# Kernel tuning notes

Measured on AMD Instinct MI355X. Metric: run time of the kernel, lower is better.

Reference implementation:

```python
import jax, jax.numpy as jnp
import numpy as np

N_NODES = 100000
N_EDGES = 1600000
IN_DIM, HID_DIM, OUT_DIM = 256, 64, 64


def gcn_conv(x, src, dst, W, b, n_nodes):
    """PyG GCNConv: D^-1/2 (A + I) D^-1/2 X W + b (self-loops added, deg on dst)."""
    h = x @ W  # [N, D_out]
    ones = jnp.ones(src.shape[0], dtype=h.dtype)
    deg = jax.ops.segment_sum(ones, dst, num_segments=n_nodes) + 1.0  # +1 for self-loop
    dinv = jax.lax.rsqrt(deg)  # deg >= 1, always finite
    norm = dinv[src] * dinv[dst]  # [E]
    # neighbor aggregation (scatter-add) + self-loop contribution
    agg = jax.ops.segment_sum(h[src] * norm[:, None], dst, num_segments=n_nodes)
    agg = agg + h * (dinv * dinv)[:, None]
    return agg + b


def gcn_backbone(x, edge_index, W1, b1, W2, b2, n_nodes):
    src, dst = edge_index[0], edge_index[1]
    h = jax.nn.relu(gcn_conv(x, src, dst, W1, b1, n_nodes))
    h = gcn_conv(h, src, dst, W2, b2, n_nodes)
    return h


def zscore(h):
    # torch .std(0) is unbiased (ddof=1)
    return (h - h.mean(axis=0)) / jnp.std(h, axis=0, ddof=1)


def setup_inputs() -> dict:
    key = jax.random.key(0)
    k = jax.random.split(key, 8)
    x1 = jax.random.normal(k[0], (N_NODES, IN_DIM), dtype=jnp.float32)
    x2 = jax.random.normal(k[1], (N_NODES, IN_DIM), dtype=jnp.float32)
    edge_index1 = jax.random.randint(k[2], (2, N_EDGES), 0, N_NODES, dtype=jnp.int64)
    edge_index2 = jax.random.randint(k[3], (2, N_EDGES), 0, N_NODES, dtype=jnp.int64)
    W1 = jax.random.normal(k[4], (IN_DIM, HID_DIM), dtype=jnp.float32) * (1.0 / np.sqrt(IN_DIM))
    b1 = jnp.zeros((HID_DIM,), dtype=jnp.float32)
    W2 = jax.random.normal(k[5], (HID_DIM, OUT_DIM), dtype=jnp.float32) * (1.0 / np.sqrt(HID_DIM))
    b2 = jnp.zeros((OUT_DIM,), dtype=jnp.float32)
    return {"x1": x1, "edge_index1": edge_index1, "x2": x2, "edge_index2": edge_index2,
            "W1": W1, "b1": b1, "W2": W2, "b2": b2}


def reference(x1, edge_index1, x2, edge_index2, W1, b1, W2, b2):
    h1 = gcn_backbone(x1, edge_index1, W1, b1, W2, b2, N_NODES)
    h2 = gcn_backbone(x2, edge_index2, W1, b1, W2, b2, N_NODES)
    return zscore(h1), zscore(h2)
```

## Files before the change

kernel.cpp:

```cpp
#include <hip/hip_runtime.h>
#include <hip/hip_bf16.h>

#define HD 64
#define CH 8192
#define BKT_SHIFT 10
#define SRC_BITS 17
#define MAXBLK 256

typedef __attribute__((ext_vector_type(8))) short bf16x8;
typedef __attribute__((ext_vector_type(4))) float f32x4;

__device__ inline unsigned short f2bf(float x) {
  unsigned u = __float_as_uint(x);
  unsigned r = u + 0x7FFF + ((u >> 16) & 1);
  return (unsigned short)(r >> 16);
}
__device__ inline float bf2f(unsigned short h) {
  return __uint_as_float(((unsigned)h) << 16);
}

__global__ __launch_bounds__(256) void k_bin1(const int* __restrict__ src0,
                                              const int* __restrict__ dst0,
                                              const int* __restrict__ src1,
                                              const int* __restrict__ dst1,
                                              int* __restrict__ tmp,
                                              int* __restrict__ counts,
                                              int* __restrict__ offsets,
                                              int NB, int NBLK, int E) {
  __shared__ int hist[128];
  __shared__ int pref[128];
  __shared__ int lofs[128];
  __shared__ int stage[CH];
  const int g = blockIdx.x / NBLK;
  const int blk = blockIdx.x % NBLK;
  const int* __restrict__ src = g ? src1 : src0;
  const int* __restrict__ dst = g ? dst1 : dst0;
  int* __restrict__ tmpg = tmp + (size_t)g * NBLK * CH;
  int* __restrict__ cntg = counts + (size_t)g * NB * NBLK;
  int* __restrict__ offg = offsets + (size_t)g * NB * NBLK;
  const int e0 = blk * CH;
  const int len = min(CH, E - e0);
  const int t = threadIdx.x;

  for (int i = t; i < 128; i += 256) hist[i] = 0;
  __syncthreads();
  int dreg[CH / 256];
#pragma unroll
  for (int it = 0; it < CH / 256; ++it) {
    int i = t + it * 256;
    if (i < len) {
      int d = dst[e0 + i];
      dreg[it] = d;
      atomicAdd(&hist[d >> BKT_SHIFT], 1);
    }
  }
  __syncthreads();
  if (t < 128) pref[t] = hist[t];
  __syncthreads();
  for (int off = 1; off < 128; off <<= 1) {
    int v = 0;
    if (t < 128 && t >= off) v = pref[t - off];
    __syncthreads();
    if (t < 128) pref[t] += v;
    __syncthreads();
  }
  if (t < NB) {
    int ex = pref[t] - hist[t];
    lofs[t] = ex;
    cntg[t * NBLK + blk] = hist[t];
    offg[t * NBLK + blk] = ex;
  }
  __syncthreads();
#pragma unroll
  for (int it = 0; it < CH / 256; ++it) {
    int i = t + it * 256;
    if (i < len) {
      int d = dreg[it], s = src[e0 + i];
      int slot = atomicAdd(&lofs[d >> BKT_SHIFT], 1);
      stage[slot] = ((d & ((1 << BKT_SHIFT) - 1)) << SRC_BITS) | s;
    }
  }
  __syncthreads();
  int nv = len >> 2;
  for (int i = t; i < nv; i += 256) ((int4*)(tmpg + e0))[i] = ((const int4*)stage)[i];
  for (int i = (nv << 2) + t; i < len; i += 256) tmpg[e0 + i] = stage[i];
}

__global__ __launch_bounds__(128) void k_bscan(const int* __restrict__ counts,
                                               int* __restrict__ bucket_base,
                                               int* __restrict__ row_start,
                                               int NB, int NBLK, int N, int E) {
  __shared__ int sh[128];
  const int g = blockIdx.x;
  const int* __restrict__ cntg = counts + (size_t)g * NB * NBLK;
  int* __restrict__ bbg = bucket_base + g * (NB + 1);
  int* __restrict__ rsg = row_start + (size_t)g * (N + 1);
  int t = threadIdx.x;
  int v = 0;
  if (t < NB) {
    const int* p = cntg + t * NBLK;
    for (int i = 0; i < NBLK; ++i) v += p[i];
  }
  sh[t] = v;
  __syncthreads();
  for (int off = 1; off < 128; off <<= 1) {
    int x = (t >= off) ? sh[t - off] : 0;
    __syncthreads();
    sh[t] += x;
    __syncthreads();
  }
  if (t < NB) bbg[t] = sh[t] - v;
  if (t == 0) {
    bbg[NB] = E;
    rsg[N] = E;
  }
}

__global__ __launch_bounds__(1024) void k_bin2m(const int* __restrict__ tmp,
                                                const int* __restrict__ counts,
                                                const int* __restrict__ offsets,
                                                const int* __restrict__ bucket_base,
                                                int* __restrict__ row_start,
                                                float* __restrict__ dinv,
                                                int* __restrict__ recs, int N, int NB,
                                                int NBLK, int E) {
  __shared__ int h[1 << BKT_SHIFT];
  __shared__ int lcur[1 << BKT_SHIFT];
  __shared__ int scnt[MAXBLK], soff[MAXBLK];
  const int g = blockIdx.x / NB;
  const int b = blockIdx.x % NB;
  const int* __restrict__ tmpg = tmp + (size_t)g * NBLK * CH;
  const int* __restrict__ cntg = counts + (size_t)g * NB * NBLK;
  const int* __restrict__ offg = offsets + (size_t)g * NB * NBLK;
  const int* __restrict__ bbg = bucket_base + g * (NB + 1);
  int* __restrict__ rsg = row_start + (size_t)g * (N + 1);
  float* __restrict__ dig = dinv + (size_t)g * N;
  int* __restrict__ recg = recs + (size_t)g * E;
  const int t = threadIdx.x;
  const int node0 = b << BKT_SHIFT;
  const int lane = t & 63, w = t >> 6;

  h[t] = 0;
  for (int i = t; i < NBLK; i += 1024) {
    scnt[i] = cntg[b * NBLK + i];
    soff[i] = offg[b * NBLK + i];
  }
  __syncthreads();
  for (int blk = w; blk < NBLK; blk += 16) {
    int cnt = scnt[blk];
    const int* p = tmpg + blk * CH + soff[blk];
    for (int j = lane; j < cnt; j += 64) atomicAdd(&h[p[j] >> SRC_BITS], 1);
  }
  __syncthreads();
  int deg = h[t];
  __syncthreads();
  for (int off = 1; off < 1024; off <<= 1) {
    int x = (t >= off) ? h[t - off] : 0;
    __syncthreads();
    h[t] += x;
    __syncthreads();
  }
  int base = bbg[b] + h[t] - deg;
  lcur[t] = base;
  int n = node0 + t;
  if (n < N) {
    rsg[n] = base;
    dig[n] = rsqrtf((float)deg + 1.0f);
  }
  __syncthreads();
  for (int blk = w; blk < NBLK; blk += 16) {
    int cnt = scnt[blk];
    const int* p = tmpg + blk * CH + soff[blk];
    for (int j = lane; j < cnt; j += 64) {
      int rec = p[j];
      int d = rec >> SRC_BITS;
      int s = rec & ((1 << SRC_BITS) - 1);
      int slot = atomicAdd(&lcur[d], 1);
      recg[slot] = s;
    }
  }
}

template <int K, int A_BF16, int B_LO>
__global__ __launch_bounds__(512, 6) void k_gemm(const void* __restrict__ Xv0,
                                                 const void* __restrict__ Xv1,
                                                 const float* __restrict__ W,
                                                 unsigned short* __restrict__ Hb, int N,
                                                 int gPer) {
  constexpr int NKS = K / 32;
  __shared__ unsigned short sBhi[NKS * 4 * 64 * 8];
  __shared__ unsigned short sBlo[B_LO ? NKS * 4 * 64 * 8 : 8];
  const int tid = threadIdx.x;
  const int g = blockIdx.x / gPer;
  const int bblk = blockIdx.x % gPer;
  const void* __restrict__ Xv = g ? Xv1 : Xv0;

  for (int idx = tid; idx < K * 64; idx += 512) {
    int k = idx >> 6, c = idx & 63;
    float wval = W[idx];
    int ks = k >> 5, r = k & 31, h2 = r >> 3, j = r & 7;
    int f = c >> 4, r16c = c & 15;
    int pos = (((ks * 4 + f) * 64) + h2 * 16 + r16c) * 8 + j;
    unsigned short hi = f2bf(wval);
    sBhi[pos] = hi;
    if (B_LO) sBlo[pos] = f2bf(wval - bf2f(hi));
  }
  __syncthreads();

  const int lane = tid & 63;
  const int wv = tid >> 6;
  const int r16 = lane & 15;
  const int half = lane >> 4;
  const int row = bblk * 128 + wv * 16 + r16;

  f32x4 acc[4];
#pragma unroll
  for (int f = 0; f < 4; ++f) acc[f] = (f32x4){0.f, 0.f, 0.f, 0.f};

#pragma unroll
  for (int ks = 0; ks < NKS; ++ks) {
    bf16x8 ahi;
    if constexpr (A_BF16) {
      union { uint4 u; bf16x8 v; } au;
      au.u = make_uint4(0, 0, 0, 0);
      if (row < N)
        au.u = *(const uint4*)((const unsigned short*)Xv + (size_t)row * K + ks * 32 + half * 8);
      ahi = au.v;
    } else {
      float4 v0 = make_float4(0.f, 0.f, 0.f, 0.f), v1 = v0;
      if (row < N) {
        const float* xp = (const float*)Xv + (size_t)row * K + ks * 32 + half * 8;
        v0 = *(const float4*)xp;
        v1 = *(const float4*)(xp + 4);
      }
      union { __hip_bfloat162 h[4]; bf16x8 v; } cu;
      cu.h[0] = __float22bfloat162_rn(make_float2(v0.x, v0.y));
      cu.h[1] = __float22bfloat162_rn(make_float2(v0.z, v0.w));
      cu.h[2] = __float22bfloat162_rn(make_float2(v1.x, v1.y));
      cu.h[3] = __float22bfloat162_rn(make_float2(v1.z, v1.w));
      ahi = cu.v;
    }
#pragma unroll
    for (int f = 0; f < 4; ++f) {
      bf16x8 bh = *(const bf16x8*)&sBhi[(((ks * 4 + f) * 64) + lane) * 8];
      acc[f] = __builtin_amdgcn_mfma_f32_16x16x32_bf16(ahi, bh, acc[f], 0, 0, 0);
      if constexpr (B_LO) {
        bf16x8 bl = *(const bf16x8*)&sBlo[(((ks * 4 + f) * 64) + lane) * 8];
        acc[f] = __builtin_amdgcn_mfma_f32_16x16x32_bf16(ahi, bl, acc[f], 0, 0, 0);
      }
    }
  }

  const int orow0 = bblk * 128 + wv * 16 + half * 4;
#pragma unroll
  for (int f = 0; f < 4; ++f) {
#pragma unroll
    for (int rg = 0; rg < 4; ++rg) {
      int orow = orow0 + rg;
      if (orow < N) Hb[((size_t)g * N + orow) * HD + f * 16 + r16] = f2bf(acc[f][rg]);
    }
  }
}

template <int OUTBF16>
__global__ __launch_bounds__(256) void k_agg(const unsigned short* __restrict__ Hb,
                                             const int* __restrict__ recs,
                                             const int* __restrict__ row_start,
                                             const float* __restrict__ dinv,
                                             const float* __restrict__ bias,
                                             void* __restrict__ outv, int N, int E,
                                             int relu) {
  const int t = threadIdx.x;
  const int nglob = (blockIdx.x * blockDim.x + t) >> 4;
  const int lane16 = t & 15;
  if (nglob >= 2 * N) return;
  const int g = nglob >= N;
  const int node = nglob - g * N;
  const int* __restrict__ rsg = row_start + (size_t)g * (N + 1);
  const int* __restrict__ R = recs + (size_t)g * E;
  const float* __restrict__ dig = dinv + (size_t)g * N;
  const unsigned short* __restrict__ Hbg = Hb + (size_t)g * N * HD;

  const int c0 = lane16 * 4;
  float di = dig[node];
  float a0, a1, a2, a3;
  {
    uint2 h = *(const uint2*)&Hbg[(size_t)node * HD + c0];
    float dd = di * di;
    a0 = bf2f((unsigned short)(h.x & 0xffff)) * dd;
    a1 = bf2f((unsigned short)(h.x >> 16)) * dd;
    a2 = bf2f((unsigned short)(h.y & 0xffff)) * dd;
    a3 = bf2f((unsigned short)(h.y >> 16)) * dd;
  }
  const int beg = rsg[node], end = rsg[node + 1];
  int e = beg;
  for (; e + 8 <= end; e += 8) {
    int s[8];
    uint2 gg[8];
    float n[8];
#pragma unroll
    for (int j = 0; j < 8; ++j) s[j] = R[e + j];
#pragma unroll
    for (int j = 0; j < 8; ++j) {
      gg[j] = *(const uint2*)&Hbg[(size_t)s[j] * HD + c0];
      n[j] = dig[s[j]];
    }
#pragma unroll
    for (int j = 0; j < 8; ++j) {
      float nn = n[j] * di;
      a0 = fmaf(bf2f((unsigned short)(gg[j].x & 0xffff)), nn, a0);
      a1 = fmaf(bf2f((unsigned short)(gg[j].x >> 16)), nn, a1);
      a2 = fmaf(bf2f((unsigned short)(gg[j].y & 0xffff)), nn, a2);
      a3 = fmaf(bf2f((unsigned short)(gg[j].y >> 16)), nn, a3);
    }
  }
  for (; e < end; ++e) {
    int s = R[e];
    uint2 gg = *(const uint2*)&Hbg[(size_t)s * HD + c0];
    float nn = dig[s] * di;
    a0 = fmaf(bf2f((unsigned short)(gg.x & 0xffff)), nn, a0);
    a1 = fmaf(bf2f((unsigned short)(gg.x >> 16)), nn, a1);
    a2 = fmaf(bf2f((unsigned short)(gg.y & 0xffff)), nn, a2);
    a3 = fmaf(bf2f((unsigned short)(gg.y >> 16)), nn, a3);
  }
  float4 bv = *(const float4*)&bias[c0];
  a0 += bv.x; a1 += bv.y; a2 += bv.z; a3 += bv.w;
  if (relu) {
    a0 = fmaxf(a0, 0.f); a1 = fmaxf(a1, 0.f);
    a2 = fmaxf(a2, 0.f); a3 = fmaxf(a3, 0.f);
  }
  if (OUTBF16) {
    uint2 o;
    o.x = ((unsigned)f2bf(a1) << 16) | f2bf(a0);
    o.y = ((unsigned)f2bf(a3) << 16) | f2bf(a2);
    *(uint2*)&((unsigned short*)outv)[(size_t)nglob * HD + c0] = o;
  } else {
    *(float4*)&((float*)outv)[(size_t)nglob * HD + c0] = make_float4(a0, a1, a2, a3);
  }
}


__global__ void k_colstats(const float* __restrict__ H, float* __restrict__ stats, int N,
                           int gridPer) {
  __shared__ float ss[256], sq[256];
  const int g = blockIdx.x / gridPer;
  const int blk = blockIdx.x % gridPer;
  const float* __restrict__ Hg = H + (size_t)g * N * HD;
  float* __restrict__ st = stats + g * 128;
  int t = threadIdx.x;
  int col = t & 63, grp = t >> 6;
  float s = 0.f, q = 0.f;
  for (int row = blk * 4 + grp; row < N; row += gridPer * 4) {
    float v = Hg[(size_t)row * HD + col];
    s += v;
    q += v * v;
  }
  ss[t] = s;
  sq[t] = q;
  __syncthreads();
  if (t < 64) {
    s = ss[t] + ss[t + 64] + ss[t + 128] + ss[t + 192];
    q = sq[t] + sq[t + 64] + sq[t + 128] + sq[t + 192];
    atomicAdd(&st[t], s);
    atomicAdd(&st[64 + t], q);
  }
}

__global__ void k_normalize(float* __restrict__ H, const float* __restrict__ stats, int N) {
  int i = blockIdx.x * blockDim.x + threadIdx.x;
  int total = 2 * N * HD;
  if (i >= total) return;
  int col = i & 63;
  const float* st = stats + (i >= N * HD ? 128 : 0);
  float sum = st[col], sumsq = st[64 + col];
  float mean = sum / (float)N;
  float var = (sumsq - sum * sum / (float)N) / (float)(N - 1);
  float r = rsqrtf(var);
  H[i] = (H[i] - mean) * r;
}


extern "C" void kernel_launch(void* const* d_in, const int* in_sizes, int n_in,
                              void* d_out, int out_size, void* d_ws, size_t ws_size,
                              hipStream_t stream) {
  const int IN_DIM = 256;
  const float* X1 = (const float*)d_in[0];
  const float* X2 = (const float*)d_in[2];
  const int* EI1 = (const int*)d_in[1];
  const int* EI2 = (const int*)d_in[3];
  const float* W1 = (const float*)d_in[4];
  const float* b1 = (const float*)d_in[5];
  const float* W2 = (const float*)d_in[6];
  const float* b2 = (const float*)d_in[7];
  const int N = in_sizes[0] / IN_DIM;
  const int E = in_sizes[1] / 2;
  const int NB = (N + (1 << BKT_SHIFT) - 1) >> BKT_SHIFT;
  const int NBLK = (E + CH - 1) / CH;

  char* ws = (char*)d_ws;
  size_t off = 0;
  auto carve = [&](size_t bytes) -> char* {
    char* p = ws + off;
    off += (bytes + 255) & ~(size_t)255;
    return p;
  };
  unsigned short* Hb = (unsigned short*)carve((size_t)2 * N * HD * 2);
  int* tmp = (int*)carve((size_t)2 * NBLK * CH * 4);
  int* recs = (int*)carve((size_t)2 * E * 4);
  char* zero_base = carve(256 * 4);
  float* stats = (float*)zero_base;
  int* row_start = (int*)carve((size_t)2 * (N + 1) * 4);
  float* dinv = (float*)carve((size_t)2 * N * 4);
  int* bucket_base = (int*)carve((size_t)2 * (NB + 1) * 4);
  int* counts = (int*)carve((size_t)2 * NB * NBLK * 4);
  int* offsets = (int*)carve((size_t)2 * NB * NBLK * 4);
  unsigned short* bufAgg = (unsigned short*)d_out;
  (void)ws_size; (void)n_in; (void)out_size;

  const int T = 256;
  const int gPer1 = (N + 127) / 128;
  const int gPer2 = (2 * N + 127) / 128;
  const int gAgg = (2 * N * 16 + T - 1) / T;
  const int gCS = 512;
  const int gElem = (2 * N * HD + T - 1) / T;

  (void)hipMemsetAsync(zero_base, 0, 256 * 4, stream);
  k_bin1<<<2 * NBLK, T, 0, stream>>>(EI1, EI1 + E, EI2, EI2 + E, tmp, counts, offsets,
                                     NB, NBLK, E);
  k_bscan<<<2, 128, 0, stream>>>(counts, bucket_base, row_start, NB, NBLK, N, E);
  k_bin2m<<<2 * NB, 1024, 0, stream>>>(tmp, counts, offsets, bucket_base, row_start,
                                       dinv, recs, N, NB, NBLK, E);

  k_gemm<256, 0, 0><<<2 * gPer1, 512, 0, stream>>>(X1, X2, W1, Hb, N, gPer1);
  k_agg<1><<<gAgg, T, 0, stream>>>(Hb, recs, row_start, dinv, b1, bufAgg, N, E, 1);
  k_gemm<64, 1, 1><<<gPer2, 512, 0, stream>>>(bufAgg, bufAgg, W2, Hb, 2 * N, gPer2);
  k_agg<0><<<gAgg, T, 0, stream>>>(Hb, recs, row_start, dinv, b2, d_out, N, E, 0);

  k_colstats<<<2 * gCS, T, 0, stream>>>((float*)d_out, stats, N, gCS);
  k_normalize<<<gElem, T, 0, stream>>>((float*)d_out, stats, N);
}
```

Baseline: 364.4 us.

## Stage GEMM A-tiles into LDS via global_load_lds with XOR swizzle

The GEMM kernel now loads X rows straight into shared memory with the direct global-to-LDS load instruction, using coalesced 16-byte chunks and an XOR swizzle to avoid bank conflicts. Previously each lane read its own strided row segments from global memory. For the fp32 input the K dimension is staged in 64-column chunks with barriers around each chunk. The occupancy hint in launch_bounds is dropped, and the extra LDS plus the barriers may lower occupancy and serialize loads against the MFMA work.

```diff
diff --git a/kernel.cpp b/kernel.cpp
--- a/kernel.cpp
+++ b/kernel.cpp
@@ -9,6 +9,13 @@
 
 typedef __attribute__((ext_vector_type(8))) short bf16x8;
 typedef __attribute__((ext_vector_type(4))) float f32x4;
+
+typedef __attribute__((address_space(1))) const unsigned int* gas_ptr;
+typedef __attribute__((address_space(3))) unsigned int* las_ptr;
+
+__device__ inline void gl_lds16(const void* g, void* l) {
+  __builtin_amdgcn_global_load_lds((gas_ptr)g, (las_ptr)l, 16, 0, 0);
+}
 
 __device__ inline unsigned short f2bf(float x) {
   unsigned u = __float_as_uint(x);
@@ -182,14 +189,16 @@
 }
 
 template <int K, int A_BF16, int B_LO>
-__global__ __launch_bounds__(512, 6) void k_gemm(const void* __restrict__ Xv0,
-                                                 const void* __restrict__ Xv1,
-                                                 const float* __restrict__ W,
-                                                 unsigned short* __restrict__ Hb, int N,
-                                                 int gPer) {
+__global__ __launch_bounds__(512) void k_gemm(const void* __restrict__ Xv0,
+                                              const void* __restrict__ Xv1,
+                                              const float* __restrict__ W,
+                                              unsigned short* __restrict__ Hb, int N,
+                                              int gPer) {
   constexpr int NKS = K / 32;
   __shared__ unsigned short sBhi[NKS * 4 * 64 * 8];
-  __shared__ unsigned short sBlo[B_LO ? NKS * 4 * 64 * 8 : 8];
+  __shared__ unsigned short sBlo[B_LO ? NKS * 4 * 64 * 8 : 4];
+  constexpr int ABYTES = A_BF16 ? (128 * K * 2) : (128 * 64 * 4);
+  __shared__ char sA[ABYTES];
   const int tid = threadIdx.x;
   const int g = blockIdx.x / gPer;
   const int bblk = blockIdx.x % gPer;
@@ -205,53 +214,84 @@
     sBhi[pos] = hi;
     if (B_LO) sBlo[pos] = f2bf(wval - bf2f(hi));
   }
-  __syncthreads();
 
   const int lane = tid & 63;
   const int wv = tid >> 6;
   const int r16 = lane & 15;
   const int half = lane >> 4;
-  const int row = bblk * 128 + wv * 16 + r16;
+  const int row0 = bblk * 128;
+  const int rowL = wv * 16 + r16;
 
   f32x4 acc[4];
 #pragma unroll
   for (int f = 0; f < 4; ++f) acc[f] = (f32x4){0.f, 0.f, 0.f, 0.f};
 
-#pragma unroll
-  for (int ks = 0; ks < NKS; ++ks) {
-    bf16x8 ahi;
-    if constexpr (A_BF16) {
-      union { uint4 u; bf16x8 v; } au;
-      au.u = make_uint4(0, 0, 0, 0);
-      if (row < N)
-        au.u = *(const uint4*)((const unsigned short*)Xv + (size_t)row * K + ks * 32 + half * 8);
-      ahi = au.v;
-    } else {
-      float4 v0 = make_float4(0.f, 0.f, 0.f, 0.f), v1 = v0;
-      if (row < N) {
-        const float* xp = (const float*)Xv + (size_t)row * K + ks * 32 + half * 8;
-        v0 = *(const float4*)xp;
-        v1 = *(const float4*)(xp + 4);
+  if constexpr (A_BF16) {
+    const unsigned short* Xb = (const unsigned short*)Xv;
+#pragma unroll
+    for (int jj = 0; jj < 2; ++jj) {
+      int slot = (wv * 2 + jj) * 64 + lane;
+      int r = slot >> 3, c = slot & 7;
+      int rr = (row0 + r < N) ? (row0 + r) : 0;
+      gl_lds16(Xb + ((size_t)rr * K + ((c ^ (r & 7)) << 3)), sA + (size_t)slot * 16);
+    }
+    __syncthreads();
+#pragma unroll
+    for (int ks = 0; ks < NKS; ++ks) {
+      int us = (ks * 4 + half) ^ (rowL & 7);
+      bf16x8 ahi = *(const bf16x8*)(sA + rowL * 128 + us * 16);
+#pragma unroll
+      for (int f = 0; f < 4; ++f) {
+        bf16x8 bh = *(const bf16x8*)&sBhi[(((ks * 4 + f) * 64) + lane) * 8];
+        acc[f] = __builtin_amdgcn_mfma_f32_16x16x32_bf16(ahi, bh, acc[f], 0, 0, 0);
+        if constexpr (B_LO) {
+          bf16x8 bl = *(const bf16x8*)&sBlo[(((ks * 4 + f) * 64) + lane) * 8];
+          acc[f] = __builtin_amdgcn_mfma_f32_16x16x32_bf16(ahi, bl, acc[f], 0, 0, 0);
+        }
       }
-      union { __hip_bfloat162 h[4]; bf16x8 v; } cu;
-      cu.h[0] = __float22bfloat162_rn(make_float2(v0.x, v0.y));
-      cu.h[1] = __float22bfloat162_rn(make_float2(v0.z, v0.w));
-      cu.h[2] = __float22bfloat162_rn(make_float2(v1.x, v1.y));
-      cu.h[3] = __float22bfloat162_rn(make_float2(v1.z, v1.w));
-      ahi = cu.v;
-    }
-#pragma unroll
-    for (int f = 0; f < 4; ++f) {
-      bf16x8 bh = *(const bf16x8*)&sBhi[(((ks * 4 + f) * 64) + lane) * 8];
-      acc[f] = __builtin_amdgcn_mfma_f32_16x16x32_bf16(ahi, bh, acc[f], 0, 0, 0);
-      if constexpr (B_LO) {
-        bf16x8 bl = *(const bf16x8*)&sBlo[(((ks * 4 + f) * 64) + lane) * 8];
-        acc[f] = __builtin_amdgcn_mfma_f32_16x16x32_bf16(ahi, bl, acc[f], 0, 0, 0);
+    }
+  } else {
+    const float* Xf = (const float*)Xv;
+#pragma unroll
+    for (int ch = 0; ch < K / 64; ++ch) {
+#pragma unroll
+      for (int jj = 0; jj < 4; ++jj) {
+        int slot = (wv * 4 + jj) * 64 + lane;
+        int r = slot >> 4, c = slot & 15;
+        int rr = (row0 + r < N) ? (row0 + r) : 0;
+        int u = c >> 1, hb = c & 1;
+        gl_lds16(Xf + ((size_t)rr * K + ch * 64 + (((u ^ (r & 7)) << 3) + (hb << 2))),
+                 sA + (size_t)slot * 16);
       }
-    }
-  }
-
-  const int orow0 = bblk * 128 + wv * 16 + half * 4;
+      __syncthreads();
+#pragma unroll
+      for (int kk = 0; kk < 2; ++kk) {
+        const int ks = ch * 2 + kk;
+        int us = (kk * 4 + half) ^ (rowL & 7);
+        const char* ap = sA + rowL * 256 + us * 32;
+        float4 a0 = *(const float4*)ap;
+        float4 a1 = *(const float4*)(ap + 16);
+        union { __hip_bfloat162 h[4]; bf16x8 v; } cu;
+        cu.h[0] = __float22bfloat162_rn(make_float2(a0.x, a0.y));
+        cu.h[1] = __float22bfloat162_rn(make_float2(a0.z, a0.w));
+        cu.h[2] = __float22bfloat162_rn(make_float2(a1.x, a1.y));
+        cu.h[3] = __float22bfloat162_rn(make_float2(a1.z, a1.w));
+        bf16x8 ahi = cu.v;
+#pragma unroll
+        for (int f = 0; f < 4; ++f) {
+          bf16x8 bh = *(const bf16x8*)&sBhi[(((ks * 4 + f) * 64) + lane) * 8];
+          acc[f] = __builtin_amdgcn_mfma_f32_16x16x32_bf16(ahi, bh, acc[f], 0, 0, 0);
+          if constexpr (B_LO) {
+            bf16x8 bl = *(const bf16x8*)&sBlo[(((ks * 4 + f) * 64) + lane) * 8];
+            acc[f] = __builtin_amdgcn_mfma_f32_16x16x32_bf16(ahi, bl, acc[f], 0, 0, 0);
+          }
+        }
+      }
+      __syncthreads();
+    }
+  }
+
+  const int orow0 = row0 + wv * 16 + half * 4;
 #pragma unroll
   for (int f = 0; f < 4; ++f) {
 #pragma unroll
```

Measured after the change: 376.8 us. +3.4%, slower.
